# Performance work log

Hardware: AMD Instinct MI355X
Metric: run time of the kernel (lower is better)

## Reference

```python
import jax, jax.numpy as jnp
import numpy as np

CHUNK = 512

def setup_inputs() -> dict:
    key = jax.random.key(0)
    kq, kk, kv = jax.random.split(key, 3)
    shape = (1, 16, 8192, 64)  # B, H, N, E
    return {
        "query": jax.random.normal(kq, shape, dtype=jnp.float32),
        "key": jax.random.normal(kk, shape, dtype=jnp.float32),
        "value": jax.random.normal(kv, shape, dtype=jnp.float32),
    }

def reference(query, key, value):
    c = CHUNK
    B, H, N, E = query.shape
    nc = N // c  # number of query chunks (N assumed divisible by c)
    scale = 1.0 / (E ** 0.5)
    neg_inf = jnp.finfo(query.dtype).min

    qc = query.reshape(B, H, nc, c, E)
    kc = key.reshape(B, H, nc, c, E)
    vc = value.reshape(B, H, nc, c, E)

    # ---- chunk 0: window is just keys[0:c], standard causal mask ----
    s0 = jnp.einsum('bhqe,bhse->bhqs', qc[:, :, 0], kc[:, :, 0]) * scale
    mask0 = jnp.triu(jnp.ones((c, c), dtype=bool), k=1)
    a0 = jax.nn.softmax(jnp.where(mask0, neg_inf, s0), axis=-1)  # (B,H,c,c)
    o0 = jnp.einsum('bhqs,bhse->bhqe', a0, vc[:, :, 0])           # (B,H,c,E)

    # ---- chunks 1..nc-1: key window = [previous chunk, current chunk] ----
    kw = jnp.concatenate([kc[:, :, :-1], kc[:, :, 1:]], axis=3)  # (B,H,nc-1,2c,E)
    vw = jnp.concatenate([vc[:, :, :-1], vc[:, :, 1:]], axis=3)
    s = jnp.einsum('bhnqe,bhnse->bhnqs', qc[:, :, 1:], kw) * scale  # (B,H,nc-1,c,2c)
    # faithful to torch.triu(ones(q_len, k_len), diagonal=1): row r keeps cols 0..r
    mask = jnp.triu(jnp.ones((c, 2 * c), dtype=bool), k=1)
    a = jax.nn.softmax(jnp.where(mask, neg_inf, s), axis=-1)        # (B,H,nc-1,c,2c)
    o = jnp.einsum('bhnqs,bhnse->bhnqe', a, vw)                     # (B,H,nc-1,c,E)

    output = jnp.concatenate([o0, o.reshape(B, H, (nc - 1) * c, E)], axis=2)  # (B,H,N,E)
    # weights concatenated along the key axis (torch cat dim=3)
    a_rest = jnp.moveaxis(a, 2, 3).reshape(B, H, c, (nc - 1) * 2 * c)
    weights = jnp.concatenate([a0, a_rest], axis=3)  # (B,H,c, c + (nc-1)*2c)
    return output, weights
```

## Files before the change

### kernel.cpp

```cpp
#include <hip/hip_runtime.h>

typedef __bf16 bf16x8 __attribute__((ext_vector_type(8)));
typedef __bf16 bf16x4 __attribute__((ext_vector_type(4)));
typedef float  f32x4  __attribute__((ext_vector_type(4)));

#define NH    16
#define SEQ   8192
#define EDIM  64
#define CHK   512
#define WCOLS 15872
#define OUT0  8388608

#define MFMA(a, b, c) __builtin_amdgcn_mfma_f32_16x16x32_bf16((a), (b), (c), 0, 0, 0)

__global__ __launch_bounds__(512, 2) void chunked_attn_kernel(
    const float* __restrict__ Qg, const float* __restrict__ Kg,
    const float* __restrict__ Vg, float* __restrict__ out)
{
    __shared__ __align__(16) __bf16 lds_k[32768];
    __shared__ __align__(16) __bf16 lds_v[32768];
    __shared__ __align__(16) __bf16 lds_p[8][2][640];

    const int tid  = threadIdx.x;
    const int lane = tid & 63;
    const int wv   = __builtin_amdgcn_readfirstlane(tid >> 6);
    const int l16  = lane & 15;
    const int quad = lane >> 4;

    const int h  = blockIdx.x >> 6;
    const int n  = (blockIdx.x >> 2) & 15;
    const int mt = blockIdx.x & 3;
    const int ns = (n == 0) ? 0 : n - 1;

    const size_t qbase = ((size_t)h * SEQ + (size_t)n  * CHK) * EDIM;
    const size_t kbase = ((size_t)h * SEQ + (size_t)ns * CHK) * EDIM;
    float* __restrict__ W = out + OUT0;
    const size_t wrow0   = (size_t)h * CHK;
    const int    colbase = (n == 0) ? 0 : (CHK + (n - 1) * 2 * CHK);

    const int m0   = mt * 128 + wv * 16;
    const int tmax = mt * 8 + wv;
    const int qrow = m0 + l16;

    const int clim = 1024 * (mt + 1);

    const float SC = 0.125f * 1.44269504088896340736f;

    #pragma unroll
    for (int it = 0; it < 8; ++it) {
        const int c = tid + it * 512;
        if (c < clim) {
            const int s = c >> 3, sub = c & 7;
            const float* src = Kg + kbase + (size_t)s * EDIM + sub * 8;
            const float4 a = *(const float4*)src;
            const float4 b = *(const float4*)(src + 4);
            bf16x8 t;
            t[0] = (__bf16)a.x; t[1] = (__bf16)a.y; t[2] = (__bf16)a.z; t[3] = (__bf16)a.w;
            t[4] = (__bf16)b.x; t[5] = (__bf16)b.y; t[6] = (__bf16)b.z; t[7] = (__bf16)b.w;
            const int idx = ((s >> 4) * 8 + sub) * 16 + (s & 15);
            ((bf16x8*)lds_k)[idx] = t;
        }
    }

    #pragma unroll
    for (int it = 0; it < 8; ++it) {
        const int c = tid + it * 512;
        if (c < clim) {
            const int e = c & 63, sb = c >> 6;
            bf16x8 t;
            #pragma unroll
            for (int j = 0; j < 8; ++j)
                t[j] = (__bf16)Vg[kbase + (size_t)(sb * 8 + j) * EDIM + e];
            const int idx = (((sb >> 2) * 4 + (e >> 4)) * 4 + (sb & 3)) * 16 + (e & 15);
            ((bf16x8*)lds_v)[idx] = t;
        }
    }

    bf16x8 aq0, aq1;
    {
        const float* qp = Qg + qbase + (size_t)(m0 + l16) * EDIM + quad * 8;
        float4 a = *(const float4*)(qp);
        float4 b = *(const float4*)(qp + 4);
        aq0[0]=(__bf16)(a.x*SC); aq0[1]=(__bf16)(a.y*SC); aq0[2]=(__bf16)(a.z*SC); aq0[3]=(__bf16)(a.w*SC);
        aq0[4]=(__bf16)(b.x*SC); aq0[5]=(__bf16)(b.y*SC); aq0[6]=(__bf16)(b.z*SC); aq0[7]=(__bf16)(b.w*SC);
        a = *(const float4*)(qp + 32);
        b = *(const float4*)(qp + 36);
        aq1[0]=(__bf16)(a.x*SC); aq1[1]=(__bf16)(a.y*SC); aq1[2]=(__bf16)(a.z*SC); aq1[3]=(__bf16)(a.w*SC);
        aq1[4]=(__bf16)(b.x*SC); aq1[5]=(__bf16)(b.y*SC); aq1[6]=(__bf16)(b.z*SC); aq1[7]=(__bf16)(b.w*SC);
    }

    if (n > 0) {
        float* const zp = W + (wrow0 + (size_t)qrow) * WCOLS + colbase + 512 + quad * 4;
        const f32x4 z = {0.f, 0.f, 0.f, 0.f};
        #pragma unroll
        for (int t = 0; t < 32; ++t)
            __builtin_nontemporal_store(z, (f32x4*)(zp + t * 16));
    }

    __syncthreads();

    const bf16x8* const kf = (const bf16x8*)lds_k;
    const bf16x8* const vf = (const bf16x8*)lds_v;

    f32x4 st[32];
    #pragma unroll
    for (int t = 0; t < 32; ++t) {
        if (t <= tmax) {
            const int kb = t * 128 + quad * 16 + l16;
            f32x4 acc = {0.f, 0.f, 0.f, 0.f};
            acc = MFMA(kf[kb],      aq0, acc);
            acc = MFMA(kf[kb + 64], aq1, acc);
            const int sb = t * 16 + quad * 4;
            #pragma unroll
            for (int r = 0; r < 4; ++r)
                acc[r] = (sb + r <= qrow) ? acc[r] : -3.0e38f;
            st[t] = acc;
        } else {
            st[t] = (f32x4){0.f, 0.f, 0.f, 0.f};
        }
    }

    float mr = -3.0e38f;
    #pragma unroll
    for (int t = 0; t < 32; ++t) {
        if (t <= tmax) {
            #pragma unroll
            for (int r = 0; r < 4; ++r) mr = fmaxf(mr, st[t][r]);
        }
    }
    mr = fmaxf(mr, __shfl_xor(mr, 16));
    mr = fmaxf(mr, __shfl_xor(mr, 32));

    float lr = 0.f;
    #pragma unroll
    for (int t = 0; t < 32; ++t) {
        if (t <= tmax) {
            #pragma unroll
            for (int r = 0; r < 4; ++r) {
                const float e = __builtin_amdgcn_exp2f(st[t][r] - mr);
                st[t][r] = e;
                lr += e;
            }
        }
    }
    lr += __shfl_xor(lr, 16);
    lr += __shfl_xor(lr, 32);
    const float ri = __builtin_amdgcn_rcpf(lr);

    #pragma unroll
    for (int t = 0; t < 32; ++t) {
        if (t <= tmax) st[t] = st[t] * ri;
    }

    {
        float* const wp = W + (wrow0 + (size_t)qrow) * WCOLS + colbase + quad * 4;
        #pragma unroll
        for (int t = 0; t < 32; ++t)
            __builtin_nontemporal_store(st[t], (f32x4*)(wp + t * 16));
    }

    f32x4 o0 = {0,0,0,0}, o1 = {0,0,0,0}, o2 = {0,0,0,0}, o3 = {0,0,0,0};
    #pragma unroll
    for (int pr = 0; pr < 16; ++pr) {
        if (2 * pr <= tmax) {
            __bf16* const pbuf = lds_p[wv][pr & 1];
            #pragma unroll
            for (int tt = 0; tt < 2; ++tt) {
                const int t = pr * 2 + tt;
                bf16x4 w;
                #pragma unroll
                for (int r = 0; r < 4; ++r) w[r] = (__bf16)st[t][r];
                *(bf16x4*)(pbuf + l16 * 40 + tt * 16 + quad * 4) = w;
            }
            const bf16x8 pa = *(const bf16x8*)(pbuf + l16 * 40 + quad * 8);
            const int vb = pr * 256 + quad * 16 + l16;
            o0 = MFMA(pa, vf[vb      ], o0);
            o1 = MFMA(pa, vf[vb +  64], o1);
            o2 = MFMA(pa, vf[vb + 128], o2);
            o3 = MFMA(pa, vf[vb + 192], o3);
        }
    }

    const int rq = m0 + quad * 4;
    const size_t ob = qbase + (size_t)rq * EDIM + l16;
    #pragma unroll
    for (int r = 0; r < 4; ++r) {
        __builtin_nontemporal_store(o0[r], out + ob + (size_t)r * EDIM     );
        __builtin_nontemporal_store(o1[r], out + ob + (size_t)r * EDIM + 16);
        __builtin_nontemporal_store(o2[r], out + ob + (size_t)r * EDIM + 32);
        __builtin_nontemporal_store(o3[r], out + ob + (size_t)r * EDIM + 48);
    }
}

extern "C" void kernel_launch(void* const* d_in, const int* in_sizes, int n_in,
                              void* d_out, int out_size, void* d_ws, size_t ws_size,
                              hipStream_t stream) {
    const float* Q = (const float*)d_in[0];
    const float* K = (const float*)d_in[1];
    const float* V = (const float*)d_in[2];
    float* out = (float*)d_out;
    chunked_attn_kernel<<<dim3(1024), dim3(512), 0, stream>>>(Q, K, V, out);
}
```

Measured before the change: 686.0 us.

## Split blocks into smaller query groups and double-buffer K/V tiles in LDS

Blocks shrink from 512 to 256 threads and cover 64 query rows instead of 128, which doubles the grid. K and V are streamed in 128-key tiles through a shared double buffer instead of staging the whole window up front, so the block needs far less LDS and more blocks can stay resident per CU. The causal mask is applied only on the diagonal tile. The costs are more barriers, K/V being loaded again by each of the extra blocks, and the weights-zeroing stores now being issued before the Q loads.

```diff
diff --git a/kernel.cpp b/kernel.cpp
--- a/kernel.cpp
+++ b/kernel.cpp
@@ -13,13 +13,12 @@
 
 #define MFMA(a, b, c) __builtin_amdgcn_mfma_f32_16x16x32_bf16((a), (b), (c), 0, 0, 0)
 
-__global__ __launch_bounds__(512, 2) void chunked_attn_kernel(
+__global__ __launch_bounds__(256, 2) void chunked_attn_kernel(
     const float* __restrict__ Qg, const float* __restrict__ Kg,
     const float* __restrict__ Vg, float* __restrict__ out)
 {
-    __shared__ __align__(16) __bf16 lds_k[32768];
-    __shared__ __align__(16) __bf16 lds_v[32768];
-    __shared__ __align__(16) __bf16 lds_p[8][2][640];
+    __shared__ __align__(16) __bf16 lds_kv[2][8192];
+    __shared__ __align__(16) __bf16 lds_p[4][2][640];
 
     const int tid  = threadIdx.x;
     const int lane = tid & 63;
@@ -27,10 +26,12 @@
     const int l16  = lane & 15;
     const int quad = lane >> 4;
 
-    const int h  = blockIdx.x >> 6;
-    const int n  = (blockIdx.x >> 2) & 15;
-    const int mt = blockIdx.x & 3;
-    const int ns = (n == 0) ? 0 : n - 1;
+    const int bid = blockIdx.x;
+    const int g   = bid >> 8;
+    const int hn  = bid & 255;
+    const int h   = hn >> 4;
+    const int n   = hn & 15;
+    const int ns  = (n == 0) ? 0 : n - 1;
 
     const size_t qbase = ((size_t)h * SEQ + (size_t)n  * CHK) * EDIM;
     const size_t kbase = ((size_t)h * SEQ + (size_t)ns * CHK) * EDIM;
@@ -38,42 +39,19 @@
     const size_t wrow0   = (size_t)h * CHK;
     const int    colbase = (n == 0) ? 0 : (CHK + (n - 1) * 2 * CHK);
 
-    const int m0   = mt * 128 + wv * 16;
-    const int tmax = mt * 8 + wv;
-    const int qrow = m0 + l16;
-
-    const int clim = 1024 * (mt + 1);
+    const int m0    = g * 64 + wv * 16;
+    const int tmax  = g * 4 + wv;
+    const int qrow  = m0 + l16;
+    const int ntile = (g + 2) >> 1;
 
     const float SC = 0.125f * 1.44269504088896340736f;
 
-    #pragma unroll
-    for (int it = 0; it < 8; ++it) {
-        const int c = tid + it * 512;
-        if (c < clim) {
-            const int s = c >> 3, sub = c & 7;
-            const float* src = Kg + kbase + (size_t)s * EDIM + sub * 8;
-            const float4 a = *(const float4*)src;
-            const float4 b = *(const float4*)(src + 4);
-            bf16x8 t;
-            t[0] = (__bf16)a.x; t[1] = (__bf16)a.y; t[2] = (__bf16)a.z; t[3] = (__bf16)a.w;
-            t[4] = (__bf16)b.x; t[5] = (__bf16)b.y; t[6] = (__bf16)b.z; t[7] = (__bf16)b.w;
-            const int idx = ((s >> 4) * 8 + sub) * 16 + (s & 15);
-            ((bf16x8*)lds_k)[idx] = t;
-        }
-    }
-
-    #pragma unroll
-    for (int it = 0; it < 8; ++it) {
-        const int c = tid + it * 512;
-        if (c < clim) {
-            const int e = c & 63, sb = c >> 6;
-            bf16x8 t;
-            #pragma unroll
-            for (int j = 0; j < 8; ++j)
-                t[j] = (__bf16)Vg[kbase + (size_t)(sb * 8 + j) * EDIM + e];
-            const int idx = (((sb >> 2) * 4 + (e >> 4)) * 4 + (sb & 3)) * 16 + (e & 15);
-            ((bf16x8*)lds_v)[idx] = t;
-        }
+    if (n > 0) {
+        float* const zp = W + (wrow0 + (size_t)qrow) * WCOLS + colbase + 512 + quad * 4;
+        const f32x4 z = {0.f, 0.f, 0.f, 0.f};
+        #pragma unroll
+        for (int t = 0; t < 32; ++t)
+            __builtin_nontemporal_store(z, (f32x4*)(zp + t * 16));
     }
 
     bf16x8 aq0, aq1;
@@ -89,34 +67,63 @@
         aq1[4]=(__bf16)(b.x*SC); aq1[5]=(__bf16)(b.y*SC); aq1[6]=(__bf16)(b.z*SC); aq1[7]=(__bf16)(b.w*SC);
     }
 
-    if (n > 0) {
-        float* const zp = W + (wrow0 + (size_t)qrow) * WCOLS + colbase + 512 + quad * 4;
-        const f32x4 z = {0.f, 0.f, 0.f, 0.f};
-        #pragma unroll
-        for (int t = 0; t < 32; ++t)
-            __builtin_nontemporal_store(z, (f32x4*)(zp + t * 16));
-    }
-
-    __syncthreads();
-
-    const bf16x8* const kf = (const bf16x8*)lds_k;
-    const bf16x8* const vf = (const bf16x8*)lds_v;
+    auto stageK = [&](int kt, int slot) {
+        #pragma unroll
+        for (int it = 0; it < 4; ++it) {
+            const int c = tid + it * 256;
+            const int s = c >> 3, sub = c & 7;
+            const float* src = Kg + kbase + (size_t)(kt * 128 + s) * EDIM + sub * 8;
+            const float4 a = *(const float4*)src;
+            const float4 b = *(const float4*)(src + 4);
+            bf16x8 t;
+            t[0] = (__bf16)a.x; t[1] = (__bf16)a.y; t[2] = (__bf16)a.z; t[3] = (__bf16)a.w;
+            t[4] = (__bf16)b.x; t[5] = (__bf16)b.y; t[6] = (__bf16)b.z; t[7] = (__bf16)b.w;
+            const int idx = ((s >> 4) * 8 + sub) * 16 + (s & 15);
+            ((bf16x8*)lds_kv[slot])[idx] = t;
+        }
+    };
+    auto stageV = [&](int kt, int slot) {
+        #pragma unroll
+        for (int it = 0; it < 4; ++it) {
+            const int c = tid + it * 256;
+            const int e = c & 63, sb = c >> 6;
+            bf16x8 t;
+            #pragma unroll
+            for (int j = 0; j < 8; ++j)
+                t[j] = (__bf16)Vg[kbase + (size_t)(kt * 128 + sb * 8 + j) * EDIM + e];
+            const int idx = (((sb >> 2) * 4 + (e >> 4)) * 4 + (sb & 3)) * 16 + (e & 15);
+            ((bf16x8*)lds_kv[slot])[idx] = t;
+        }
+    };
 
     f32x4 st[32];
     #pragma unroll
-    for (int t = 0; t < 32; ++t) {
-        if (t <= tmax) {
-            const int kb = t * 128 + quad * 16 + l16;
-            f32x4 acc = {0.f, 0.f, 0.f, 0.f};
-            acc = MFMA(kf[kb],      aq0, acc);
-            acc = MFMA(kf[kb + 64], aq1, acc);
-            const int sb = t * 16 + quad * 4;
-            #pragma unroll
-            for (int r = 0; r < 4; ++r)
-                acc[r] = (sb + r <= qrow) ? acc[r] : -3.0e38f;
-            st[t] = acc;
-        } else {
-            st[t] = (f32x4){0.f, 0.f, 0.f, 0.f};
+    for (int t = 0; t < 32; ++t) st[t] = (f32x4){0.f, 0.f, 0.f, 0.f};
+
+    stageK(0, 0);
+    #pragma unroll
+    for (int kt = 0; kt < 4; ++kt) {
+        if (kt < ntile) {
+            __syncthreads();
+            if (kt + 1 < ntile) stageK(kt + 1, (kt + 1) & 1);
+            const bf16x8* const kf = (const bf16x8*)lds_kv[kt & 1];
+            #pragma unroll
+            for (int tt = 0; tt < 8; ++tt) {
+                const int t = kt * 8 + tt;
+                if (t <= tmax) {
+                    const int kb = tt * 128 + quad * 16 + l16;
+                    f32x4 acc = {0.f, 0.f, 0.f, 0.f};
+                    acc = MFMA(kf[kb],      aq0, acc);
+                    acc = MFMA(kf[kb + 64], aq1, acc);
+                    if (t == tmax) {
+                        const int sb = t * 16 + quad * 4;
+                        #pragma unroll
+                        for (int r = 0; r < 4; ++r)
+                            acc[r] = (sb + r <= qrow) ? acc[r] : -3.0e38f;
+                    }
+                    st[t] = acc;
+                }
+            }
         }
     }
 
@@ -148,9 +155,7 @@
     const float ri = __builtin_amdgcn_rcpf(lr);
 
     #pragma unroll
-    for (int t = 0; t < 32; ++t) {
-        if (t <= tmax) st[t] = st[t] * ri;
-    }
+    for (int t = 0; t < 32; ++t) st[t] = st[t] * ri;
 
     {
         float* const wp = W + (wrow0 + (size_t)qrow) * WCOLS + colbase + quad * 4;
@@ -159,25 +164,37 @@
             __builtin_nontemporal_store(st[t], (f32x4*)(wp + t * 16));
     }
 
+    __syncthreads();
+    stageV(0, 0);
+
     f32x4 o0 = {0,0,0,0}, o1 = {0,0,0,0}, o2 = {0,0,0,0}, o3 = {0,0,0,0};
     #pragma unroll
-    for (int pr = 0; pr < 16; ++pr) {
-        if (2 * pr <= tmax) {
-            __bf16* const pbuf = lds_p[wv][pr & 1];
-            #pragma unroll
-            for (int tt = 0; tt < 2; ++tt) {
-                const int t = pr * 2 + tt;
-                bf16x4 w;
-                #pragma unroll
-                for (int r = 0; r < 4; ++r) w[r] = (__bf16)st[t][r];
-                *(bf16x4*)(pbuf + l16 * 40 + tt * 16 + quad * 4) = w;
+    for (int kt = 0; kt < 4; ++kt) {
+        if (kt < ntile) {
+            __syncthreads();
+            if (kt + 1 < ntile) stageV(kt + 1, (kt + 1) & 1);
+            const bf16x8* const vf = (const bf16x8*)lds_kv[kt & 1];
+            #pragma unroll
+            for (int pq = 0; pq < 4; ++pq) {
+                const int pr = kt * 4 + pq;
+                if (2 * pr <= tmax) {
+                    __bf16* const pbuf = lds_p[wv][pq & 1];
+                    #pragma unroll
+                    for (int tt = 0; tt < 2; ++tt) {
+                        const int t = pr * 2 + tt;
+                        bf16x4 w;
+                        #pragma unroll
+                        for (int r = 0; r < 4; ++r) w[r] = (__bf16)st[t][r];
+                        *(bf16x4*)(pbuf + l16 * 40 + tt * 16 + quad * 4) = w;
+                    }
+                    const bf16x8 pa = *(const bf16x8*)(pbuf + l16 * 40 + quad * 8);
+                    const int vb = pq * 256 + quad * 16 + l16;
+                    o0 = MFMA(pa, vf[vb      ], o0);
+                    o1 = MFMA(pa, vf[vb +  64], o1);
+                    o2 = MFMA(pa, vf[vb + 128], o2);
+                    o3 = MFMA(pa, vf[vb + 192], o3);
+                }
             }
-            const bf16x8 pa = *(const bf16x8*)(pbuf + l16 * 40 + quad * 8);
-            const int vb = pr * 256 + quad * 16 + l16;
-            o0 = MFMA(pa, vf[vb      ], o0);
-            o1 = MFMA(pa, vf[vb +  64], o1);
-            o2 = MFMA(pa, vf[vb + 128], o2);
-            o3 = MFMA(pa, vf[vb + 192], o3);
         }
     }
 
@@ -199,5 +216,5 @@
     const float* K = (const float*)d_in[1];
     const float* V = (const float*)d_in[2];
     float* out = (float*)d_out;
-    chunked_attn_kernel<<<dim3(1024), dim3(512), 0, stream>>>(Q, K, V, out);
+    chunked_attn_kernel<<<dim3(2048), dim3(256), 0, stream>>>(Q, K, V, out);
 }
```

After: 681.3 us. Within noise of the previous version (-0.7%).
